# Performance work log

Measured on AMD Instinct MI355X. Metric: run time of the kernel, lower is better.

The kernel has to match this reference:

```python
import jax, jax.numpy as jnp
import numpy as np
from jax import lax

H = W = 512
NT = 1000


def setup_inputs() -> dict:
    key = jax.random.key(0)
    kx, ky = jax.random.split(key)
    X = jax.random.uniform(kx, (H, W), dtype=jnp.float32)
    Y = jax.random.uniform(ky, (H, W), dtype=jnp.float32)
    return {"X": X, "Y": Y}


def reference(X, Y):
    # Gaussian initial condition, same math as torch.exp(-50*((X-0.5)^2+(Y-0.5)^2))
    x0 = jnp.exp(-50.0 * ((X - 0.5) ** 2 + (Y - 0.5) ** 2))
    h, w = x0.shape
    # mask zeroing the boundary (rows/cols 0 and -1)
    mask = jnp.zeros((h, w), dtype=x0.dtype).at[1:-1, 1:-1].set(1.0)

    def step(x, _):
        # 3x3 cross kernel [[0,.25,0],[.25,0,.25],[0,.25,0]] with zero padding=1,
        # expressed as four shifted adds (identical math, no conv launch overhead)
        p = jnp.pad(x, 1)
        xn = 0.25 * (p[:-2, 1:-1] + p[2:, 1:-1] + p[1:-1, :-2] + p[1:-1, 2:])
        return xn * mask, None

    x, _ = lax.scan(step, x0, None, length=NT)
    # original returns NCHW with N=C=1
    return x[None, None]
```

## Files before the change

kernel.cpp:

```cpp
#include <hip/hip_runtime.h>
#include <math.h>


#define HW 512
#define NP 64
#define NC 32

__device__ __forceinline__ int mode_of(int p) {
    return (p < NC) ? (p + 1) : (p + 447);
}

__device__ __forceinline__ float gauss(const float* __restrict__ X,
                                       const float* __restrict__ Y, int idx) {
    float dx = X[idx] - 0.5f, dy = Y[idx] - 0.5f;
    return expf(-50.0f * (dx * dx + dy * dy));
}

__global__ void k_prep(const float* __restrict__ X, const float* __restrict__ Y,
                       float* __restrict__ x1, float* __restrict__ S,
                       float* __restrict__ ST) {
    int b = blockIdx.x, t = threadIdx.x;
    if (b < 1024) {
        int idx = b * 256 + t;
        int i = idx >> 9, j = idx & 511;
        float v = 0.0f;
        if (i > 0 && i < HW - 1 && j > 0 && j < HW - 1) {
            v = 0.25f * (gauss(X, Y, idx - HW) + gauss(X, Y, idx + HW) +
                         gauss(X, Y, idx - 1)  + gauss(X, Y, idx + 1));
        }
        x1[idx] = v;
    } else {
        int idx = (b - 1024) * 256 + t;
        int pa = idx >> 9, i = idx & 511;
        long tt = ((long)(pa + 1) * (long)i) % 1022;
        float s = (float)sin((double)tt * (M_PI / 511.0));
        S[pa * HW + i] = s;
        ST[i * NC + pa] = s;
    }
}

__global__ void k_m1(const float* __restrict__ S, const float* __restrict__ x1,
                     float* __restrict__ P) {
    int j = blockIdx.x * 256 + threadIdx.x;
    int pa0 = blockIdx.y * 8;
    int iz = blockIdx.z;
    int i0 = iz * 16;
    const float* Sb = S + pa0 * HW + i0;
    const float* xp = x1 + i0 * HW + j;
    float ae[8] = {0.f, 0.f, 0.f, 0.f, 0.f, 0.f, 0.f, 0.f};
    float ao[8] = {0.f, 0.f, 0.f, 0.f, 0.f, 0.f, 0.f, 0.f};
    #pragma unroll
    for (int i = 0; i < 16; i++) {
        float x = xp[i * HW];
        if ((i & 1) == 0) {
            #pragma unroll
            for (int k = 0; k < 8; k++) ae[k] += Sb[k * HW + i] * x;
        } else {
            #pragma unroll
            for (int k = 0; k < 8; k++) ao[k] += Sb[k * HW + i] * x;
        }
    }
    float* Pp = P + iz * NP * HW + j;
    #pragma unroll
    for (int k = 0; k < 8; k++) {
        Pp[(pa0 + k) * HW]      = ae[k] + ao[k];
        Pp[(63 - pa0 - k) * HW] = ao[k] - ae[k];
    }
}

__global__ void k_m23(const float* __restrict__ P, const float* __restrict__ ST,
                      const float* __restrict__ S, float* __restrict__ E) {
    __shared__ float c1[HW];
    __shared__ float pe[512], po[512];
    __shared__ float dp[NC], dm[NC];
    int p = blockIdx.x, t = threadIdx.x;
    {
        const float* Pp = P + p * HW + t;
        float s0 = 0.f, s1 = 0.f, s2 = 0.f, s3 = 0.f;
        #pragma unroll
        for (int iz = 0; iz < 32; iz += 4) {
            s0 += Pp[(iz + 0) * NP * HW];
            s1 += Pp[(iz + 1) * NP * HW];
            s2 += Pp[(iz + 2) * NP * HW];
            s3 += Pp[(iz + 3) * NP * HW];
        }
        c1[t] = (s0 + s1) + (s2 + s3);
    }
    __syncthreads();
    int qa = t & 31, jg = t >> 5;
    {
        const float* STp = ST + (jg * 32) * NC + qa;
        const float* cc = c1 + jg * 32;
        float be = 0.f, bo = 0.f;
        #pragma unroll
        for (int jj = 0; jj < 32; jj += 2) {
            be += cc[jj] * STp[jj * NC];
            bo += cc[jj + 1] * STp[(jj + 1) * NC];
        }
        pe[t] = be;
        po[t] = bo;
    }
    __syncthreads();
    if (t < NC) {
        float se = 0.f, so = 0.f;
        #pragma unroll
        for (int g = 0; g < 16; g++) {
            se += pe[g * 32 + t];
            so += po[g * 32 + t];
        }
        float dlo = se + so;
        float dhi = so - se;
        double lp = cos((double)mode_of(p) * M_PI / 511.0);
        double ca = cos((double)(t + 1) * M_PI / 511.0);
        double lam1 = 0.5 * (lp + ca);
        double lam2 = 0.5 * (lp - ca);
        double r1 = 1.0, b1 = fabs(lam1);
        double r2 = 1.0, b2 = fabs(lam2);
        int e = 999;
        #pragma unroll
        for (int k = 0; k < 10; k++) {
            if (e & 1) { r1 *= b1; r2 *= b2; }
            b1 *= b1; b2 *= b2;
            e >>= 1;
        }
        if (lam1 < 0.0) r1 = -r1;
        if (lam2 < 0.0) r2 = -r2;
        const double sc = (2.0 / 511.0) * (2.0 / 511.0);
        dlo *= (float)(r1 * sc);
        dhi *= (float)(r2 * sc);
        dp[t] = dlo + dhi;
        dm[t] = dlo - dhi;
    }
    __syncthreads();
    const float* sel = (t & 1) ? dp : dm;
    float e0 = 0.f, e1 = 0.f;
    #pragma unroll
    for (int q2 = 0; q2 < NC; q2 += 2) {
        e0 += sel[q2] * S[q2 * HW + t];
        e1 += sel[q2 + 1] * S[(q2 + 1) * HW + t];
    }
    E[p * HW + t] = e0 + e1;
}

__global__ void k_m4(const float* __restrict__ S, const float* __restrict__ E,
                     float* __restrict__ out) {
    int j = blockIdx.x * 256 + threadIdx.x;
    int i0 = blockIdx.y * 4;
    float a0 = 0.f, a1 = 0.f, a2 = 0.f, a3 = 0.f;
    #pragma unroll 8
    for (int pa = 0; pa < NC; pa++) {
        float elo = E[pa * HW + j];
        float ehi = E[(63 - pa) * HW + j];
        float ep = elo + ehi, em = elo - ehi;
        const float* Sp = S + pa * HW + i0;
        a0 += Sp[0] * em;
        a1 += Sp[1] * ep;
        a2 += Sp[2] * em;
        a3 += Sp[3] * ep;
    }
    out[(i0 + 0) * HW + j] = a0;
    out[(i0 + 1) * HW + j] = a1;
    out[(i0 + 2) * HW + j] = a2;
    out[(i0 + 3) * HW + j] = a3;
}


extern "C" void kernel_launch(void* const* d_in, const int* in_sizes, int n_in,
                              void* d_out, int out_size, void* d_ws, size_t ws_size,
                              hipStream_t stream) {
    const float* X = (const float*)d_in[0];
    const float* Y = (const float*)d_in[1];
    float* out = (float*)d_out;

    float* ws = (float*)d_ws;
    float* x1 = ws;
    float* S  = x1 + HW * HW;
    float* ST = S + NC * HW;
    float* E  = ST + HW * NC;
    float* P  = E + NP * HW;

    k_prep<<<dim3(1088),        dim3(256), 0, stream>>>(X, Y, x1, S, ST);
    k_m1  <<<dim3(2, 4, 32),    dim3(256), 0, stream>>>(S, x1, P);
    k_m23 <<<dim3(NP),          dim3(512), 0, stream>>>(P, ST, S, E);
    k_m4  <<<dim3(2, 128),      dim3(256), 0, stream>>>(S, E, out);
}
```

Before: 70.60 us.

## Fuse initial-condition stencil and sine basis generation into first projection kernel

Merges the prep kernel into the first spectral projection kernel. Each block computes the Gaussian on a haloed tile in shared memory, applies the first stencil step there, and builds its sine coefficients locally, so the x1 intermediate round-trip and one launch go away. In exchange, each tile's Gaussian is recomputed by the 4 pa-blocks that share it, and each block now does expf and double-precision sin work before its projection.

```diff
diff --git a/kernel.cpp b/kernel.cpp
--- a/kernel.cpp
+++ b/kernel.cpp
@@ -5,59 +5,62 @@
 #define HW 512
 #define NP 64
 #define NC 32
+#define TIW 258
 
 __device__ __forceinline__ int mode_of(int p) {
     return (p < NC) ? (p + 1) : (p + 447);
 }
 
-__device__ __forceinline__ float gauss(const float* __restrict__ X,
-                                       const float* __restrict__ Y, int idx) {
-    float dx = X[idx] - 0.5f, dy = Y[idx] - 0.5f;
-    return expf(-50.0f * (dx * dx + dy * dy));
-}
-
-__global__ void k_prep(const float* __restrict__ X, const float* __restrict__ Y,
-                       float* __restrict__ x1, float* __restrict__ S,
-                       float* __restrict__ ST) {
-    int b = blockIdx.x, t = threadIdx.x;
-    if (b < 1024) {
-        int idx = b * 256 + t;
-        int i = idx >> 9, j = idx & 511;
-        float v = 0.0f;
-        if (i > 0 && i < HW - 1 && j > 0 && j < HW - 1) {
-            v = 0.25f * (gauss(X, Y, idx - HW) + gauss(X, Y, idx + HW) +
-                         gauss(X, Y, idx - 1)  + gauss(X, Y, idx + 1));
-        }
-        x1[idx] = v;
-    } else {
-        int idx = (b - 1024) * 256 + t;
-        int pa = idx >> 9, i = idx & 511;
-        long tt = ((long)(pa + 1) * (long)i) % 1022;
-        float s = (float)sin((double)tt * (M_PI / 511.0));
-        S[pa * HW + i] = s;
-        ST[i * NC + pa] = s;
-    }
-}
-
-__global__ void k_m1(const float* __restrict__ S, const float* __restrict__ x1,
-                     float* __restrict__ P) {
-    int j = blockIdx.x * 256 + threadIdx.x;
+__global__ void k_a(const float* __restrict__ X, const float* __restrict__ Y,
+                    float* __restrict__ S, float* __restrict__ ST,
+                    float* __restrict__ P) {
+    __shared__ float gT[18][TIW];
+    __shared__ float sA[8][16];
+    int t = threadIdx.x;
+    int jb = blockIdx.x * 256;
     int pa0 = blockIdx.y * 8;
     int iz = blockIdx.z;
     int i0 = iz * 16;
-    const float* Sb = S + pa0 * HW + i0;
-    const float* xp = x1 + i0 * HW + j;
+    for (int e = t; e < 18 * TIW; e += 256) {
+        int r = e / TIW, c = e - r * TIW;
+        int gi = i0 - 1 + r;
+        int gj = jb - 1 + c;
+        gi = min(max(gi, 0), HW - 1);
+        gj = min(max(gj, 0), HW - 1);
+        int idx = gi * HW + gj;
+        float dx = X[idx] - 0.5f, dy = Y[idx] - 0.5f;
+        gT[r][c] = expf(-50.0f * (dx * dx + dy * dy));
+    }
+    if (t < 128) {
+        int k = t >> 4, ii = t & 15;
+        int pa = pa0 + k, i = i0 + ii;
+        long tt = ((long)(pa + 1) * (long)i) % 1022;
+        float s = (float)sin((double)tt * (M_PI / 511.0));
+        sA[k][ii] = s;
+        if (blockIdx.x == 0) {
+            S[pa * HW + i] = s;
+            ST[i * NC + pa] = s;
+        }
+    }
+    __syncthreads();
+    int j = jb + t;
+    bool jin = (j > 0) && (j < HW - 1);
     float ae[8] = {0.f, 0.f, 0.f, 0.f, 0.f, 0.f, 0.f, 0.f};
     float ao[8] = {0.f, 0.f, 0.f, 0.f, 0.f, 0.f, 0.f, 0.f};
     #pragma unroll
-    for (int i = 0; i < 16; i++) {
-        float x = xp[i * HW];
-        if ((i & 1) == 0) {
+    for (int ii = 0; ii < 16; ii++) {
+        int i = i0 + ii;
+        float xv = 0.0f;
+        if (jin && i > 0 && i < HW - 1) {
+            xv = 0.25f * (gT[ii][t + 1] + gT[ii + 2][t + 1] +
+                          gT[ii + 1][t] + gT[ii + 1][t + 2]);
+        }
+        if ((ii & 1) == 0) {
             #pragma unroll
-            for (int k = 0; k < 8; k++) ae[k] += Sb[k * HW + i] * x;
+            for (int k = 0; k < 8; k++) ae[k] += sA[k][ii] * xv;
         } else {
             #pragma unroll
-            for (int k = 0; k < 8; k++) ao[k] += Sb[k * HW + i] * x;
+            for (int k = 0; k < 8; k++) ao[k] += sA[k][ii] * xv;
         }
     }
     float* Pp = P + iz * NP * HW + j;
@@ -173,14 +176,12 @@
     float* out = (float*)d_out;
 
     float* ws = (float*)d_ws;
-    float* x1 = ws;
-    float* S  = x1 + HW * HW;
+    float* S  = ws;
     float* ST = S + NC * HW;
     float* E  = ST + HW * NC;
     float* P  = E + NP * HW;
 
-    k_prep<<<dim3(1088),        dim3(256), 0, stream>>>(X, Y, x1, S, ST);
-    k_m1  <<<dim3(2, 4, 32),    dim3(256), 0, stream>>>(S, x1, P);
+    k_a   <<<dim3(2, 4, 32),    dim3(256), 0, stream>>>(X, Y, S, ST, P);
     k_m23 <<<dim3(NP),          dim3(512), 0, stream>>>(P, ST, S, E);
     k_m4  <<<dim3(2, 128),      dim3(256), 0, stream>>>(S, E, out);
 }
```

After: 71.52 us. Within noise of the previous version (+1.3%).
